# Performance work log

Hardware: AMD Instinct MI355X
Metric: run time of the kernel (lower is better)

## Reference

```python
import jax, jax.numpy as jnp
import numpy as np

M, N, B, L = 512, 2048, 4, 20
H_DENSITY = 0.02  # Tanner graph sparsity: row weight ~N*p=40, col weight ~M*p=10


def setup_inputs() -> dict:
    key = jax.random.key(0)
    ks = jax.random.split(key, 10)
    H = jax.random.bernoulli(ks[0], H_DENSITY, (M, N)).astype(jnp.float32)
    llrs = jax.random.uniform(ks[1], (N,), jnp.float32)
    syndromes = jax.random.randint(ks[2], (B, M, 1), 0, 2, jnp.int32)
    errors = jax.random.randint(ks[3], (B, N), 0, 2, jnp.int32)
    weights_de = jax.random.uniform(ks[4], (L, M, N), jnp.float32)
    weights_llr = jax.random.uniform(ks[5], (L, N), jnp.float32)
    marg_weights_de = jax.random.uniform(ks[6], (L, M, N), jnp.float32)
    marg_weights_llr = jax.random.uniform(ks[7], (L, N), jnp.float32)
    rhos = jnp.ones((L,), jnp.float32)
    residual_weights = jnp.zeros((L,), jnp.float32)
    return dict(syndromes=syndromes, errors=errors, H=H, llrs=llrs,
                weights_de=weights_de, weights_llr=weights_llr,
                marg_weights_de=marg_weights_de, marg_weights_llr=marg_weights_llr,
                rhos=rhos, residual_weights=residual_weights)


def reference(syndromes, errors, H, llrs, weights_de, weights_llr,
              marg_weights_de, marg_weights_llr, rhos, residual_weights):
    batch = syndromes.shape[0]
    m, n = H.shape
    rhos_norm = jax.nn.softmax(rhos)                       # (L,)
    sign = 1.0 - 2.0 * syndromes.astype(H.dtype)           # (B,m,1): (-1)**syndrome
    err_f = errors.astype(H.dtype)                         # (B,n)
    eps = 1e-6

    def step(msgs_dn, xs):
        w_de, w_llr, mw_de, mw_llr, rho, rw = xs
        # error-node (variable) update: column-sum minus self, masked by H
        msgs_en = (H * (llrs * w_llr)
                   + jnp.sum(msgs_dn * w_de, axis=1, keepdims=True)) * H - msgs_dn
        # detector-node (check) update: tanh-product rule with self-exclusion
        d = jnp.tanh(msgs_en * 0.5)
        d = jnp.where(d == 0, jnp.asarray(1.0, d.dtype), d)
        d = jnp.clip(d, -1.0 + eps, 1.0 - eps)
        row_prod = jnp.prod(d, axis=2, keepdims=True)      # (B,m,1)
        msgs_new = 2.0 * jnp.arctanh(row_prod / d) * (sign * H) + rw * msgs_dn
        # marginal beliefs and weighted BCE loss
        beliefs = jnp.sum(msgs_new * mw_de, axis=1) + llrs * mw_llr   # (B,n)
        loss_b = jnp.sum(jax.nn.softplus(beliefs) - (1.0 - err_f) * beliefs, axis=1)
        return msgs_new, rho * loss_b

    init = jnp.zeros((batch, m, n), H.dtype)
    _, losses = jax.lax.scan(
        step, init,
        (weights_de, weights_llr, marg_weights_de, marg_weights_llr,
         rhos_norm, residual_weights))
    return jnp.sum(losses) / batch
```

## Files before the change

### kernel.cpp

```cpp
#include <hip/hip_runtime.h>

#define MM 512
#define NN 2048
#define BB 4
#define LL 20
#define MAXDEG 128
#define EMAX  24576
#define NT    1024
#define RR    8
#define ROWSB 64
#define SLOTS 4096
#define COLSB 256
#define EPSV  1e-6f

#define WS_ROW_DEG   0
#define WS_ROW_PAD   2048
#define WS_ROW_OFFF  264192
#define WS_ROW_PTR   266240
#define WS_EDGE_CSR  268416
#define WS_WDE_P     366720
#define WS_MWDE_P    2988160
#define WS_COLPART   5609600
#define WS_BELPART   6133888
#define WS_BAR       6658176

__global__ __launch_bounds__(64)
void build_rows(const float* __restrict__ H, int* __restrict__ row_deg,
                int* __restrict__ row_pad, float* __restrict__ row_offf) {
    int i = blockIdx.x, lane = threadIdx.x;
    const float* hrow = H + (size_t)i * NN;
    int base = 0;
    for (int chunk = 0; chunk < NN / 64; ++chunk) {
        int c = chunk * 64 + lane;
        bool pred = hrow[c] != 0.0f;
        unsigned long long mask = __ballot(pred);
        int before = __popcll(mask & ((1ull << lane) - 1ull));
        if (pred) {
            int idx = base + before;
            if (idx < MAXDEG) row_pad[i * MAXDEG + idx] = c;
        }
        base += __popcll(mask);
    }
    if (lane == 0) {
        row_deg[i] = base < MAXDEG ? base : MAXDEG;
        row_offf[i] = powf(1.0f - EPSV, (float)(NN - base));
    }
}

__global__ __launch_bounds__(512)
void scan_rows(const int* __restrict__ row_deg, int* __restrict__ row_ptr) {
    __shared__ int tmp[512];
    int t = threadIdx.x;
    tmp[t] = row_deg[t];
    __syncthreads();
    for (int off = 1; off < 512; off <<= 1) {
        int v = (t >= off) ? tmp[t - off] : 0;
        __syncthreads();
        tmp[t] += v;
        __syncthreads();
    }
    if (t == 0) row_ptr[0] = 0;
    row_ptr[t + 1] = tmp[t];
}

__global__ __launch_bounds__(64)
void fill_csr(const int* __restrict__ row_deg, const int* __restrict__ row_pad,
              const int* __restrict__ row_ptr, unsigned* __restrict__ edge_csr) {
    int i = blockIdx.x, lane = threadIdx.x;
    int deg = row_deg[i], base = row_ptr[i];
    for (int k = lane; k < deg; k += 64)
        edge_csr[base + k] = ((unsigned)i << 16) | (unsigned)row_pad[i * MAXDEG + k];
}

__global__ __launch_bounds__(256)
void gather_weights(const float* __restrict__ w_de, const float* __restrict__ mw_de,
                    const unsigned* __restrict__ edge_csr, const int* __restrict__ row_ptr,
                    float* __restrict__ wde_p, float* __restrict__ mwde_p) {
    int idx = blockIdx.x * 256 + threadIdx.x;
    int l = idx / (RR * SLOTS);
    int rem = idx - l * (RR * SLOTS);
    int r = rem / SLOTS, s = rem - r * SLOTS;
    int e = row_ptr[r * ROWSB] + s;
    if (e < row_ptr[(r + 1) * ROWSB]) {
        unsigned pk = edge_csr[e];
        size_t src = (size_t)l * MM * NN + (size_t)(pk >> 16) * NN + (pk & 0xffffu);
        wde_p[idx]  = w_de[src];
        mwde_p[idx] = mw_de[src];
    } else {
        wde_p[idx]  = 0.0f;
        mwde_p[idx] = 0.0f;
    }
}

__device__ __forceinline__ void grid_barrier(int* ctr) {
    __syncthreads();
    if (threadIdx.x == 0) {
        __threadfence();
        __hip_atomic_fetch_add(ctr, 1, __ATOMIC_RELAXED, __HIP_MEMORY_SCOPE_AGENT);
        while (__hip_atomic_load(ctr, __ATOMIC_RELAXED, __HIP_MEMORY_SCOPE_AGENT) < RR)
            __builtin_amdgcn_s_sleep(1);
        __threadfence();
    }
    __syncthreads();
}

__global__ __launch_bounds__(NT, 4)
void nbp_main(const int* __restrict__ synd, const int* __restrict__ errs,
              const float* __restrict__ llrs,
              const float* __restrict__ w_llr, const float* __restrict__ mw_llr,
              const float* __restrict__ rhos, const float* __restrict__ resw,
              const int* __restrict__ row_ptr, const float* __restrict__ row_offf,
              const unsigned* __restrict__ edge_csr,
              const float* __restrict__ wde_p, const float* __restrict__ mwde_p,
              float* __restrict__ colpart, float* __restrict__ belpart,
              int* __restrict__ bar, float* __restrict__ out) {
    __shared__ float d_sb[SLOTS];
    __shared__ float colsum_s[NN];
    __shared__ float bel_s[NN];
    __shared__ float ncs_s[NN];
    __shared__ float llrs_s[NN];
    __shared__ float rowprod_s[ROWSB];
    __shared__ float rp_coef[ROWSB];
    __shared__ int   rowptr_s[ROWSB + 1];
    __shared__ float rho_n[LL];
    __shared__ float red[16];

    const int blk = blockIdx.x;
    const int b = blk & 3, r = blk >> 2;
    const int i0 = r * ROWSB;
    const int tid = threadIdx.x;
    const int lane = tid & 63, wave = tid >> 6;

    int* bar_b = bar + b * 64;

    if (tid == 0) {
        float mx = -1e30f;
        for (int l = 0; l < LL; ++l) mx = fmaxf(mx, rhos[l]);
        float s = 0.0f;
        for (int l = 0; l < LL; ++l) { float e = __expf(rhos[l] - mx); rho_n[l] = e; s += e; }
        for (int l = 0; l < LL; ++l) rho_n[l] /= s;
    }
    if (tid < ROWSB) {
        int i = i0 + tid;
        rowptr_s[tid] = row_ptr[i];
        rp_coef[tid] = row_offf[i] * (1.0f - 2.0f * (float)synd[b * MM + i]);
    }
    if (tid == ROWSB) rowptr_s[ROWSB] = row_ptr[i0 + ROWSB];
    for (int j = tid; j < NN; j += NT) {
        float lj = llrs[j];
        llrs_s[j] = lj;
        colsum_s[j] = lj * w_llr[j];
    }

    const int e_lo = row_ptr[i0], e_hi = row_ptr[i0 + ROWSB];
    const int cnt = e_hi - e_lo;
    const int s0 = 4 * tid;

    unsigned idx[4];
    float msg[4], d_r[4];
    #pragma unroll
    for (int k = 0; k < 4; ++k) {
        int e = e_lo + s0 + k;
        idx[k] = edge_csr[(s0 + k) < cnt ? e : e_lo] - ((unsigned)i0 << 16);
        msg[k] = 0.0f;
    }
    __syncthreads();

    float loss = 0.0f;

    for (int l = 0; l < LL; ++l) {
        const float rw = resw[l];
        const int par = l & 1;
        float* colpart_b = colpart + ((size_t)par * BB + b) * RR * NN;
        float* belpart_b = belpart + ((size_t)par * BB + b) * RR * NN;

        const float4 mq = *(const float4*)(mwde_p + ((size_t)(l * RR + r) * SLOTS) + s0);
        float4 wq = make_float4(0.f, 0.f, 0.f, 0.f);
        if (l + 1 < LL)
            wq = *(const float4*)(wde_p + ((size_t)((l + 1) * RR + r) * SLOTS) + s0);
        const float mv[4] = {mq.x, mq.y, mq.z, mq.w};
        const float wn[4] = {wq.x, wq.y, wq.z, wq.w};

        #pragma unroll
        for (int k = 0; k < 4; ++k) {
            int j = idx[k] & 0xffffu;
            float en = colsum_s[j] - msg[k];
            float t = __expf(en);
            float d = 1.0f - 2.0f * __builtin_amdgcn_rcpf(t + 1.0f);
            if (d == 0.0f) d = 1.0f;
            d = fminf(fmaxf(d, -1.0f + EPSV), 1.0f - EPSV);
            d_r[k] = d;
        }
        *(float4*)&d_sb[s0] = make_float4(d_r[0], d_r[1], d_r[2], d_r[3]);
        __syncthreads();

        if (tid < 4 * ROWSB) {
            int i = tid >> 2, q = tid & 3;
            int s = rowptr_s[i] - e_lo;
            int deg = rowptr_s[i + 1] - rowptr_s[i];
            float p = 1.0f;
            for (int c = q; c < deg; c += 4) p *= d_sb[s + c];
            p *= __shfl_xor(p, 1);
            p *= __shfl_xor(p, 2);
            if (q == 0) rowprod_s[i] = p * rp_coef[i];
        } else {
            for (int j = tid - 4 * ROWSB; j < NN; j += NT - 4 * ROWSB) {
                bel_s[j] = 0.0f;
                ncs_s[j] = 0.0f;
            }
        }
        __syncthreads();

        #pragma unroll
        for (int k = 0; k < 4; ++k) {
            int il = idx[k] >> 16;
            int j  = idx[k] & 0xffffu;
            float rq = rowprod_s[il] * __builtin_amdgcn_rcpf(d_r[k]);
            float v = __logf(1.0f + rq) - __logf(1.0f - rq) + rw * msg[k];
            msg[k] = v;
            if (s0 + k < cnt) {
                atomicAdd(&bel_s[j], v * mv[k]);
                if (l + 1 < LL) atomicAdd(&ncs_s[j], v * wn[k]);
            }
        }
        __syncthreads();
        for (int j = tid; j < NN; j += NT) {
            belpart_b[r * NN + j] = bel_s[j];
            colpart_b[r * NN + j] = ncs_s[j];
        }
        grid_barrier(&bar_b[l]);

        if (tid < COLSB) {
            int j = r * COLSB + tid;
            float bel = llrs_s[j] * mw_llr[l * NN + j];
            const float* bp = belpart_b + j;
            #pragma unroll
            for (int r2 = 0; r2 < RR; ++r2) bel += bp[r2 * NN];
            float sp = fmaxf(bel, 0.0f) + log1pf(__expf(-fabsf(bel)));
            loss += rho_n[l] * (sp - (1.0f - (float)errs[b * NN + j]) * bel);
        }
        if (l + 1 < LL) {
            const float* wl_next = w_llr + (l + 1) * NN;
            for (int j = tid; j < NN; j += NT) {
                float s = llrs_s[j] * wl_next[j];
                const float* cp = colpart_b + j;
                #pragma unroll
                for (int r2 = 0; r2 < RR; ++r2) s += cp[r2 * NN];
                colsum_s[j] = s;
            }
        }
        __syncthreads();
    }

    #pragma unroll
    for (int off = 32; off > 0; off >>= 1) loss += __shfl_down(loss, off);
    if (lane == 0) red[wave] = loss;
    __syncthreads();
    if (wave == 0) {
        float v = (lane < 16) ? red[lane] : 0.0f;
        #pragma unroll
        for (int off = 8; off > 0; off >>= 1) v += __shfl_down(v, off);
        if (lane == 0) atomicAdd(out, v * 0.25f);
    }
}

extern "C" void kernel_launch(void* const* d_in, const int* in_sizes, int n_in,
                              void* d_out, int out_size, void* d_ws, size_t ws_size,
                              hipStream_t stream) {
    const int*   synd  = (const int*)  d_in[0];
    const int*   errs  = (const int*)  d_in[1];
    const float* H     = (const float*)d_in[2];
    const float* llrs  = (const float*)d_in[3];
    const float* w_de  = (const float*)d_in[4];
    const float* w_llr = (const float*)d_in[5];
    const float* mw_de = (const float*)d_in[6];
    const float* mw_llr= (const float*)d_in[7];
    const float* rhos  = (const float*)d_in[8];
    const float* resw  = (const float*)d_in[9];

    char* ws = (char*)d_ws;
    int*      row_deg  = (int*)     (ws + WS_ROW_DEG);
    int*      row_pad  = (int*)     (ws + WS_ROW_PAD);
    float*    row_offf = (float*)   (ws + WS_ROW_OFFF);
    int*      row_ptr  = (int*)     (ws + WS_ROW_PTR);
    unsigned* edge_csr = (unsigned*)(ws + WS_EDGE_CSR);
    float*    wde_p    = (float*)   (ws + WS_WDE_P);
    float*    mwde_p   = (float*)   (ws + WS_MWDE_P);
    float*    colpart  = (float*)   (ws + WS_COLPART);
    float*    belpart  = (float*)   (ws + WS_BELPART);
    int*      bar      = (int*)     (ws + WS_BAR);
    float*    out      = (float*)d_out;

    hipMemsetAsync(bar, 0, BB * 64 * sizeof(int), stream);
    hipMemsetAsync(d_out, 0, sizeof(float), stream);

    build_rows<<<MM, 64, 0, stream>>>(H, row_deg, row_pad, row_offf);
    scan_rows<<<1, 512, 0, stream>>>(row_deg, row_ptr);
    fill_csr<<<MM, 64, 0, stream>>>(row_deg, row_pad, row_ptr, edge_csr);
    gather_weights<<<(LL * RR * SLOTS) / 256, 256, 0, stream>>>(w_de, mw_de, edge_csr,
                                                                row_ptr, wde_p, mwde_p);
    nbp_main<<<BB * RR, NT, 0, stream>>>(synd, errs, llrs, w_llr, mw_llr, rhos, resw,
                                         row_ptr, row_offf, edge_csr, wde_p, mwde_p,
                                         colpart, belpart, bar, out);
}
```

Before: 452.9 us.

## Run one block per batch item, drop grid barriers and global partial sums

Replaces the 32-block decomposition (8 row-groups per batch item, synchronised with a spin-wait grid barrier and global column/belief partial buffers) with a single 1024-thread block per batch item that holds all edges, 24 per thread, in registers. Row products are computed per thread as segmented partials written to shared memory and then combined per row, so the cross-block atomic barrier and global round-trips disappear. The cost is far less parallelism (4 blocks on a large GPU) and much higher register pressure per thread. build_rows also preloads its H row into registers before the ballot loop.

```diff
diff --git a/kernel.cpp b/kernel.cpp
--- a/kernel.cpp
+++ b/kernel.cpp
@@ -7,10 +7,8 @@
 #define MAXDEG 128
 #define EMAX  24576
 #define NT    1024
-#define RR    8
-#define ROWSB 64
-#define SLOTS 4096
-#define COLSB 256
+#define EPT   24
+#define PMAX  8
 #define EPSV  1e-6f
 
 #define WS_ROW_DEG   0
@@ -19,25 +17,25 @@
 #define WS_ROW_PTR   266240
 #define WS_EDGE_CSR  268416
 #define WS_WDE_P     366720
-#define WS_MWDE_P    2988160
-#define WS_COLPART   5609600
-#define WS_BELPART   6133888
-#define WS_BAR       6658176
+#define WS_MWDE_P    2332800
 
 __global__ __launch_bounds__(64)
 void build_rows(const float* __restrict__ H, int* __restrict__ row_deg,
                 int* __restrict__ row_pad, float* __restrict__ row_offf) {
     int i = blockIdx.x, lane = threadIdx.x;
     const float* hrow = H + (size_t)i * NN;
+    float v[32];
+    #pragma unroll
+    for (int c = 0; c < 32; ++c) v[c] = hrow[c * 64 + lane];
     int base = 0;
-    for (int chunk = 0; chunk < NN / 64; ++chunk) {
-        int c = chunk * 64 + lane;
-        bool pred = hrow[c] != 0.0f;
+    #pragma unroll
+    for (int c = 0; c < 32; ++c) {
+        bool pred = v[c] != 0.0f;
         unsigned long long mask = __ballot(pred);
         int before = __popcll(mask & ((1ull << lane) - 1ull));
         if (pred) {
-            int idx = base + before;
-            if (idx < MAXDEG) row_pad[i * MAXDEG + idx] = c;
+            int k = base + before;
+            if (k < MAXDEG) row_pad[i * MAXDEG + k] = c * 64 + lane;
         }
         base += __popcll(mask);
     }
@@ -77,13 +75,11 @@
                     const unsigned* __restrict__ edge_csr, const int* __restrict__ row_ptr,
                     float* __restrict__ wde_p, float* __restrict__ mwde_p) {
     int idx = blockIdx.x * 256 + threadIdx.x;
-    int l = idx / (RR * SLOTS);
-    int rem = idx - l * (RR * SLOTS);
-    int r = rem / SLOTS, s = rem - r * SLOTS;
-    int e = row_ptr[r * ROWSB] + s;
-    if (e < row_ptr[(r + 1) * ROWSB]) {
+    int l = idx / EMAX, e = idx - l * EMAX;
+    int E = row_ptr[MM];
+    if (e < E) {
         unsigned pk = edge_csr[e];
-        size_t src = (size_t)l * MM * NN + (size_t)(pk >> 16) * NN + (pk & 0xffffu);
+        size_t src = (size_t)l * (MM * NN) + (size_t)(pk >> 16) * NN + (pk & 0xffffu);
         wde_p[idx]  = w_de[src];
         mwde_p[idx] = mw_de[src];
     } else {
@@ -92,19 +88,7 @@
     }
 }
 
-__device__ __forceinline__ void grid_barrier(int* ctr) {
-    __syncthreads();
-    if (threadIdx.x == 0) {
-        __threadfence();
-        __hip_atomic_fetch_add(ctr, 1, __ATOMIC_RELAXED, __HIP_MEMORY_SCOPE_AGENT);
-        while (__hip_atomic_load(ctr, __ATOMIC_RELAXED, __HIP_MEMORY_SCOPE_AGENT) < RR)
-            __builtin_amdgcn_s_sleep(1);
-        __threadfence();
-    }
-    __syncthreads();
-}
-
-__global__ __launch_bounds__(NT, 4)
+__global__ __launch_bounds__(NT)
 void nbp_main(const int* __restrict__ synd, const int* __restrict__ errs,
               const float* __restrict__ llrs,
               const float* __restrict__ w_llr, const float* __restrict__ mw_llr,
@@ -112,26 +96,21 @@
               const int* __restrict__ row_ptr, const float* __restrict__ row_offf,
               const unsigned* __restrict__ edge_csr,
               const float* __restrict__ wde_p, const float* __restrict__ mwde_p,
-              float* __restrict__ colpart, float* __restrict__ belpart,
-              int* __restrict__ bar, float* __restrict__ out) {
-    __shared__ float d_sb[SLOTS];
+              float* __restrict__ out) {
     __shared__ float colsum_s[NN];
     __shared__ float bel_s[NN];
     __shared__ float ncs_s[NN];
-    __shared__ float llrs_s[NN];
-    __shared__ float rowprod_s[ROWSB];
-    __shared__ float rp_coef[ROWSB];
-    __shared__ int   rowptr_s[ROWSB + 1];
+    __shared__ float partial_s[PMAX * MM];
+    __shared__ float rowprod_s[MM];
+    __shared__ float rp_coef[MM];
+    __shared__ int   rowptr_s[MM + 1];
     __shared__ float rho_n[LL];
     __shared__ float red[16];
 
-    const int blk = blockIdx.x;
-    const int b = blk & 3, r = blk >> 2;
-    const int i0 = r * ROWSB;
+    const int b = blockIdx.x;
     const int tid = threadIdx.x;
     const int lane = tid & 63, wave = tid >> 6;
-
-    int* bar_b = bar + b * 64;
+    const int s0 = EPT * tid;
 
     if (tid == 0) {
         float mx = -1e30f;
@@ -140,28 +119,30 @@
         for (int l = 0; l < LL; ++l) { float e = __expf(rhos[l] - mx); rho_n[l] = e; s += e; }
         for (int l = 0; l < LL; ++l) rho_n[l] /= s;
     }
-    if (tid < ROWSB) {
-        int i = i0 + tid;
-        rowptr_s[tid] = row_ptr[i];
-        rp_coef[tid] = row_offf[i] * (1.0f - 2.0f * (float)synd[b * MM + i]);
-    }
-    if (tid == ROWSB) rowptr_s[ROWSB] = row_ptr[i0 + ROWSB];
-    for (int j = tid; j < NN; j += NT) {
-        float lj = llrs[j];
-        llrs_s[j] = lj;
-        colsum_s[j] = lj * w_llr[j];
-    }
-
-    const int e_lo = row_ptr[i0], e_hi = row_ptr[i0 + ROWSB];
-    const int cnt = e_hi - e_lo;
-    const int s0 = 4 * tid;
-
-    unsigned idx[4];
-    float msg[4], d_r[4];
-    #pragma unroll
-    for (int k = 0; k < 4; ++k) {
-        int e = e_lo + s0 + k;
-        idx[k] = edge_csr[(s0 + k) < cnt ? e : e_lo] - ((unsigned)i0 << 16);
+    if (tid < MM) {
+        rowptr_s[tid] = row_ptr[tid];
+        rp_coef[tid] = row_offf[tid] * (1.0f - 2.0f * (float)synd[b * MM + tid]);
+    }
+    if (tid == MM) rowptr_s[MM] = row_ptr[MM];
+
+    const int j0 = tid, j1 = tid + NT;
+    const float llr0 = llrs[j0], llr1 = llrs[j1];
+    const float ef0 = 1.0f - (float)errs[b * NN + j0];
+    const float ef1 = 1.0f - (float)errs[b * NN + j1];
+    colsum_s[j0] = llr0 * w_llr[j0];
+    colsum_s[j1] = llr1 * w_llr[j1];
+    bel_s[j0] = 0.0f; bel_s[j1] = 0.0f;
+    ncs_s[j0] = 0.0f; ncs_s[j1] = 0.0f;
+
+    int cnt = row_ptr[MM];
+    if (cnt > EMAX) cnt = EMAX;
+
+    unsigned idx[EPT];
+    float msg[EPT], d_r[EPT];
+    #pragma unroll
+    for (int k = 0; k < EPT; ++k) {
+        int e = s0 + k;
+        idx[k] = edge_csr[e < cnt ? e : (cnt - 1)];
         msg[k] = 0.0f;
     }
     __syncthreads();
@@ -170,19 +151,34 @@
 
     for (int l = 0; l < LL; ++l) {
         const float rw = resw[l];
-        const int par = l & 1;
-        float* colpart_b = colpart + ((size_t)par * BB + b) * RR * NN;
-        float* belpart_b = belpart + ((size_t)par * BB + b) * RR * NN;
-
-        const float4 mq = *(const float4*)(mwde_p + ((size_t)(l * RR + r) * SLOTS) + s0);
-        float4 wq = make_float4(0.f, 0.f, 0.f, 0.f);
-        if (l + 1 < LL)
-            wq = *(const float4*)(wde_p + ((size_t)((l + 1) * RR + r) * SLOTS) + s0);
-        const float mv[4] = {mq.x, mq.y, mq.z, mq.w};
-        const float wn[4] = {wq.x, wq.y, wq.z, wq.w};
+        const bool last = (l + 1 == LL);
+
+        float mv[EPT], wn[EPT];
+        {
+            const float4* mp = (const float4*)(mwde_p + (size_t)l * EMAX + s0);
+            #pragma unroll
+            for (int q = 0; q < EPT / 4; ++q) {
+                float4 t4 = mp[q];
+                mv[4*q] = t4.x; mv[4*q+1] = t4.y; mv[4*q+2] = t4.z; mv[4*q+3] = t4.w;
+            }
+            if (!last) {
+                const float4* wp = (const float4*)(wde_p + (size_t)(l + 1) * EMAX + s0);
+                #pragma unroll
+                for (int q = 0; q < EPT / 4; ++q) {
+                    float4 t4 = wp[q];
+                    wn[4*q] = t4.x; wn[4*q+1] = t4.y; wn[4*q+2] = t4.z; wn[4*q+3] = t4.w;
+                }
+            } else {
+                #pragma unroll
+                for (int k = 0; k < EPT; ++k) wn[k] = 0.0f;
+            }
+        }
+        float mwl0 = mw_llr[l * NN + j0], mwl1 = mw_llr[l * NN + j1];
+        float wl0 = 0.0f, wl1 = 0.0f;
+        if (!last) { wl0 = w_llr[(l + 1) * NN + j0]; wl1 = w_llr[(l + 1) * NN + j1]; }
 
         #pragma unroll
-        for (int k = 0; k < 4; ++k) {
+        for (int k = 0; k < EPT; ++k) {
             int j = idx[k] & 0xffffu;
             float en = colsum_s[j] - msg[k];
             float t = __expf(en);
@@ -191,28 +187,37 @@
             d = fminf(fmaxf(d, -1.0f + EPSV), 1.0f - EPSV);
             d_r[k] = d;
         }
-        *(float4*)&d_sb[s0] = make_float4(d_r[0], d_r[1], d_r[2], d_r[3]);
-        __syncthreads();
-
-        if (tid < 4 * ROWSB) {
-            int i = tid >> 2, q = tid & 3;
-            int s = rowptr_s[i] - e_lo;
-            int deg = rowptr_s[i + 1] - rowptr_s[i];
+        if (s0 < cnt) {
+            int crow = idx[0] >> 16;
+            int q = tid - rowptr_s[crow] / EPT;
             float p = 1.0f;
-            for (int c = q; c < deg; c += 4) p *= d_sb[s + c];
-            p *= __shfl_xor(p, 1);
-            p *= __shfl_xor(p, 2);
-            if (q == 0) rowprod_s[i] = p * rp_coef[i];
-        } else {
-            for (int j = tid - 4 * ROWSB; j < NN; j += NT - 4 * ROWSB) {
-                bel_s[j] = 0.0f;
-                ncs_s[j] = 0.0f;
-            }
+            #pragma unroll
+            for (int k = 0; k < EPT; ++k) {
+                int rk = idx[k] >> 16;
+                if (rk != crow) {
+                    partial_s[q * MM + crow] = p;
+                    crow = rk; q = 0; p = 1.0f;
+                }
+                if (s0 + k < cnt) p *= d_r[k];
+            }
+            partial_s[q * MM + crow] = p;
+        }
+        __syncthreads();
+
+        if (tid < MM) {
+            int lo = rowptr_s[tid], hi = rowptr_s[tid + 1];
+            float p = 1.0f;
+            if (hi > lo) {
+                int f = lo / EPT;
+                int span = (hi - 1) / EPT - f + 1;
+                for (int q = 0; q < span; ++q) p *= partial_s[q * MM + tid];
+            }
+            rowprod_s[tid] = p * rp_coef[tid];
         }
         __syncthreads();
 
         #pragma unroll
-        for (int k = 0; k < 4; ++k) {
+        for (int k = 0; k < EPT; ++k) {
             int il = idx[k] >> 16;
             int j  = idx[k] & 0xffffu;
             float rq = rowprod_s[il] * __builtin_amdgcn_rcpf(d_r[k]);
@@ -220,33 +225,22 @@
             msg[k] = v;
             if (s0 + k < cnt) {
                 atomicAdd(&bel_s[j], v * mv[k]);
-                if (l + 1 < LL) atomicAdd(&ncs_s[j], v * wn[k]);
-            }
-        }
-        __syncthreads();
-        for (int j = tid; j < NN; j += NT) {
-            belpart_b[r * NN + j] = bel_s[j];
-            colpart_b[r * NN + j] = ncs_s[j];
-        }
-        grid_barrier(&bar_b[l]);
-
-        if (tid < COLSB) {
-            int j = r * COLSB + tid;
-            float bel = llrs_s[j] * mw_llr[l * NN + j];
-            const float* bp = belpart_b + j;
-            #pragma unroll
-            for (int r2 = 0; r2 < RR; ++r2) bel += bp[r2 * NN];
-            float sp = fmaxf(bel, 0.0f) + log1pf(__expf(-fabsf(bel)));
-            loss += rho_n[l] * (sp - (1.0f - (float)errs[b * NN + j]) * bel);
-        }
-        if (l + 1 < LL) {
-            const float* wl_next = w_llr + (l + 1) * NN;
-            for (int j = tid; j < NN; j += NT) {
-                float s = llrs_s[j] * wl_next[j];
-                const float* cp = colpart_b + j;
-                #pragma unroll
-                for (int r2 = 0; r2 < RR; ++r2) s += cp[r2 * NN];
-                colsum_s[j] = s;
+                if (!last) atomicAdd(&ncs_s[j], v * wn[k]);
+            }
+        }
+        __syncthreads();
+
+        {
+            float bel0 = llr0 * mwl0 + bel_s[j0];
+            float bel1 = llr1 * mwl1 + bel_s[j1];
+            bel_s[j0] = 0.0f; bel_s[j1] = 0.0f;
+            float sp0 = fmaxf(bel0, 0.0f) + log1pf(__expf(-fabsf(bel0)));
+            float sp1 = fmaxf(bel1, 0.0f) + log1pf(__expf(-fabsf(bel1)));
+            loss += rho_n[l] * ((sp0 - ef0 * bel0) + (sp1 - ef1 * bel1));
+            if (!last) {
+                colsum_s[j0] = llr0 * wl0 + ncs_s[j0];
+                colsum_s[j1] = llr1 * wl1 + ncs_s[j1];
+                ncs_s[j0] = 0.0f; ncs_s[j1] = 0.0f;
             }
         }
         __syncthreads();
@@ -286,20 +280,15 @@
     unsigned* edge_csr = (unsigned*)(ws + WS_EDGE_CSR);
     float*    wde_p    = (float*)   (ws + WS_WDE_P);
     float*    mwde_p   = (float*)   (ws + WS_MWDE_P);
-    float*    colpart  = (float*)   (ws + WS_COLPART);
-    float*    belpart  = (float*)   (ws + WS_BELPART);
-    int*      bar      = (int*)     (ws + WS_BAR);
     float*    out      = (float*)d_out;
 
-    hipMemsetAsync(bar, 0, BB * 64 * sizeof(int), stream);
     hipMemsetAsync(d_out, 0, sizeof(float), stream);
 
     build_rows<<<MM, 64, 0, stream>>>(H, row_deg, row_pad, row_offf);
     scan_rows<<<1, 512, 0, stream>>>(row_deg, row_ptr);
     fill_csr<<<MM, 64, 0, stream>>>(row_deg, row_pad, row_ptr, edge_csr);
-    gather_weights<<<(LL * RR * SLOTS) / 256, 256, 0, stream>>>(w_de, mw_de, edge_csr,
-                                                                row_ptr, wde_p, mwde_p);
-    nbp_main<<<BB * RR, NT, 0, stream>>>(synd, errs, llrs, w_llr, mw_llr, rhos, resw,
-                                         row_ptr, row_offf, edge_csr, wde_p, mwde_p,
-                                         colpart, belpart, bar, out);
-}
+    gather_weights<<<(LL * EMAX) / 256, 256, 0, stream>>>(w_de, mw_de, edge_csr,
+                                                          row_ptr, wde_p, mwde_p);
+    nbp_main<<<BB, NT, 0, stream>>>(synd, errs, llrs, w_llr, mw_llr, rhos, resw,
+                                    row_ptr, row_offf, edge_csr, wde_p, mwde_p, out);
+}
```

Measured after the change: 1.509 ms. +233.2%, slower.
